# Kernel tuning notes

Hardware: AMD Instinct MI355X
Metric: run time of the kernel (lower is better)

The kernel has to match this reference:

```python
import jax, jax.numpy as jnp
import numpy as np

N_HEAD = 16


def setup_inputs() -> dict:
    key = jax.random.key(0)
    ks = jax.random.split(key, 6)
    B, T, C = 8, 1024, 1024
    s = 0.02
    return {
        "x": jax.random.normal(ks[0], (B, T, C), dtype=jnp.float32),
        "Wk": jax.random.normal(ks[1], (C, C), dtype=jnp.float32) * s,
        "bk": jnp.zeros((C,), dtype=jnp.float32),
        "Wq": jax.random.normal(ks[2], (C, C), dtype=jnp.float32) * s,
        "bq": jnp.zeros((C,), dtype=jnp.float32),
        "Wv": jax.random.normal(ks[3], (C, C), dtype=jnp.float32) * s,
        "bv": jnp.zeros((C,), dtype=jnp.float32),
        "Wp": jax.random.normal(ks[4], (C, C), dtype=jnp.float32) * s,
        "bp": jnp.zeros((C,), dtype=jnp.float32),
    }


def reference(x, Wk, bk, Wq, bq, Wv, bv, Wp, bp):
    B, T, C = x.shape
    H = N_HEAD
    d = C // H
    # QKV projections, split heads -> [B, H, T, d]
    k = (x @ Wk + bk).reshape(B, T, H, d).transpose(0, 2, 1, 3)
    q = (x @ Wq + bq).reshape(B, T, H, d).transpose(0, 2, 1, 3)
    v = (x @ Wv + bv).reshape(B, T, H, d).transpose(0, 2, 1, 3)
    # NOTE: original computes K @ Q^T (not Q @ K^T) and scales by C^-0.5
    attn = jnp.einsum('bhid,bhjd->bhij', k, q) * (C ** -0.5)
    mask = jnp.tril(jnp.ones((T, T), dtype=bool))  # tril==0 positions masked
    attn = jnp.where(mask, attn, -jnp.inf)
    attn = jax.nn.softmax(attn, axis=-1)
    out = jnp.einsum('bhij,bhjd->bhid', attn, v)  # [B, H, T, d]
    out = out.transpose(0, 2, 1, 3).reshape(B, T, C)
    return out @ Wp + bp
```

## Files before the change

### kernel.cpp

```cpp
#include <hip/hip_runtime.h>

typedef unsigned short u16;
typedef unsigned int u32;
typedef __bf16 bf16x8 __attribute__((ext_vector_type(8)));
typedef float f32x4 __attribute__((ext_vector_type(4)));

__device__ __forceinline__ u16 f2bf(float f) {
  u32 u = __builtin_bit_cast(u32, f);
  u += 0x7fffu + ((u >> 16) & 1u);
  return (u16)(u >> 16);
}

#define GLOAD_LDS16(g, l) __builtin_amdgcn_global_load_lds( \
    (const __attribute__((address_space(1))) void*)(g),     \
    (__attribute__((address_space(3))) void*)(l), 16, 0, 0)

#define SCK (0.03125f * 1.44269504088896f)

#define BARF() do { asm volatile("" ::: "memory"); \
                    __builtin_amdgcn_s_barrier();  \
                    asm volatile("" ::: "memory"); } while (0)

__global__ __launch_bounds__(256) void prep_k(const float* __restrict__ x,
                                              const float* __restrict__ W0,
                                              const float* __restrict__ W1,
                                              const float* __restrict__ W2,
                                              const float* __restrict__ W3,
                                              u16* __restrict__ xb,
                                              u16* __restrict__ WT) {
  __shared__ float tile[64][65];
  const int tid = threadIdx.x;
  if (blockIdx.x < 4096) {
    size_t i = (size_t)blockIdx.x * 256 + tid;
    const float4* p = reinterpret_cast<const float4*>(x) + i * 2;
    float4 a = p[0], b = p[1];
    u32 w0 = f2bf(a.x) | ((u32)f2bf(a.y) << 16);
    u32 w1 = f2bf(a.z) | ((u32)f2bf(a.w) << 16);
    u32 w2 = f2bf(b.x) | ((u32)f2bf(b.y) << 16);
    u32 w3 = f2bf(b.z) | ((u32)f2bf(b.w) << 16);
    uint4 o; o.x = w0; o.y = w1; o.z = w2; o.w = w3;
    *reinterpret_cast<uint4*>(xb + i * 8) = o;
    return;
  }
  const int bid2 = blockIdx.x - 4096;
  const int z = bid2 >> 8, kt = bid2 & 15, nt = (bid2 >> 4) & 15;
  const float* W = z == 0 ? W0 : z == 1 ? W1 : z == 2 ? W2 : W3;
  u16* dst = WT + (size_t)z * 1024 * 1024;
  const int k0 = kt * 64, n0 = nt * 64;
  const int rr = tid >> 4, c4 = (tid & 15) * 4;
#pragma unroll
  for (int p = 0; p < 4; ++p) {
    int r = rr + p * 16;
    float4 v = *reinterpret_cast<const float4*>(W + (size_t)(k0 + r) * 1024 + n0 + c4);
    tile[r][c4 + 0] = v.x; tile[r][c4 + 1] = v.y;
    tile[r][c4 + 2] = v.z; tile[r][c4 + 3] = v.w;
  }
  __syncthreads();
#pragma unroll
  for (int p = 0; p < 4; ++p) {
    int nl = rr + p * 16;
    u32 w0 = f2bf(tile[c4 + 0][nl]) | ((u32)f2bf(tile[c4 + 1][nl]) << 16);
    u32 w1 = f2bf(tile[c4 + 2][nl]) | ((u32)f2bf(tile[c4 + 3][nl]) << 16);
    uint2 o; o.x = w0; o.y = w1;
    *reinterpret_cast<uint2*>(dst + (size_t)(n0 + nl) * 1024 + k0 + c4) = o;
  }
}

template <int MODE>
__global__ __launch_bounds__(512, 2) void gemm8_k(
    const u16* __restrict__ A, const u16* __restrict__ BT,
    const float* __restrict__ bias0, const float* __restrict__ bias1,
    const float* __restrict__ bias2,
    u16* __restrict__ out_k, u16* __restrict__ out_q, u16* __restrict__ out_vT,
    float* __restrict__ out_f) {
  constexpr int BN = (MODE == 0) ? 192 : 128;
  constexpr int NB = BN / 64;
  constexpr int LPT = 4 + NB;
  constexpr int WCW = BN / 4;
  constexpr int HALF = 8 + NB;

  __shared__ __align__(16) u16 As[2][256 * 64];
  __shared__ __align__(16) u16 Bs[2][BN * 64];

  const int tid = threadIdx.x;
  const int w = tid >> 6, lane = tid & 63;
  const int wr = w >> 2, wc = w & 3;
  const int fr = lane & 15, fq = lane >> 4;
  const int d = fr & 7;

  const int bid = (int)blockIdx.x;
  const int xcd = bid & 7, c = bid >> 3;
  int bx, by;
  if constexpr (MODE == 0) {
    bx = (xcd & 3) * 8 + (c >> 3);
    by = (xcd >> 2) * 8 + (c & 7);
  } else {
    bx = xcd * 4 + (c >> 3);
    by = c & 7;
  }
  const int row0 = bx * 256, col0 = by * BN;

  const int r0 = tid >> 3;
  const int cbg = (tid & 7) ^ (r0 & 7);
  const u16* Asrc = A + (size_t)(row0 + r0) * 1024 + cbg * 8;
  const u16* Bsrc = BT + (size_t)(col0 + r0) * 1024 + cbg * 8;

#define STAGE8(buf, t) do {                                                  \
    _Pragma("unroll")                                                        \
    for (int sw = 0; sw < 4; ++sw)                                           \
      GLOAD_LDS16(Asrc + (size_t)sw * 65536 + (t) * 64,                      \
                  &As[buf][sw * 4096 + tid * 8]);                            \
    _Pragma("unroll")                                                        \
    for (int sw = 0; sw < NB; ++sw)                                          \
      GLOAD_LDS16(Bsrc + (size_t)sw * 65536 + (t) * 64,                      \
                  &Bs[buf][sw * 4096 + tid * 8]);                            \
  } while (0)

#define AOFF(mb, kk) ((wr * 128 + (mb) * 16 + fr) * 128 + (((((kk) << 2) | fq) ^ d) << 4))
#define BOFF(nb, kk) ((wc * WCW + (nb) * 16 + fr) * 128 + (((((kk) << 2) | fq) ^ d) << 4))

  f32x4 acc[8][NB] = {};

  STAGE8(0, 0);
  STAGE8(1, 1);
  asm volatile("s_waitcnt vmcnt(%0)" :: "n"(LPT) : "memory");
  BARF();

#pragma unroll 1
  for (int g = 0; g < 16; ++g) {
    const int buf = g & 1;
    const char* Ac = (const char*)&As[buf][0];
    const char* Bc = (const char*)&Bs[buf][0];
    bf16x8 a[8][2], b[NB][2];

#pragma unroll
    for (int mb = 0; mb < 8; ++mb) a[mb][0] = *(const bf16x8*)(Ac + AOFF(mb, 0));
#pragma unroll
    for (int nb = 0; nb < NB; ++nb) b[nb][0] = *(const bf16x8*)(Bc + BOFF(nb, 0));
#pragma unroll
    for (int mb = 0; mb < 8; ++mb) a[mb][1] = *(const bf16x8*)(Ac + AOFF(mb, 1));
#pragma unroll
    for (int nb = 0; nb < NB; ++nb) b[nb][1] = *(const bf16x8*)(Bc + BOFF(nb, 1));

    asm volatile("s_waitcnt lgkmcnt(%0)" :: "n"(HALF) : "memory");
    __builtin_amdgcn_s_setprio(1);
#pragma unroll
    for (int mb = 0; mb < 8; ++mb)
#pragma unroll
      for (int nb = 0; nb < NB; ++nb)
        acc[mb][nb] = __builtin_amdgcn_mfma_f32_16x16x32_bf16(
            a[mb][0], b[nb][0], acc[mb][nb], 0, 0, 0);
    __builtin_amdgcn_s_setprio(0);

    asm volatile("s_waitcnt lgkmcnt(0)" ::: "memory");
    BARF();
    if (g + 2 < 16) STAGE8(buf, g + 2);

    __builtin_amdgcn_s_setprio(1);
#pragma unroll
    for (int mb = 0; mb < 8; ++mb)
#pragma unroll
      for (int nb = 0; nb < NB; ++nb)
        acc[mb][nb] = __builtin_amdgcn_mfma_f32_16x16x32_bf16(
            a[mb][1], b[nb][1], acc[mb][nb], 0, 0, 0);
    __builtin_amdgcn_s_setprio(0);

    if (g <= 13)      asm volatile("s_waitcnt vmcnt(%0)" :: "n"(LPT) : "memory");
    else if (g == 14) asm volatile("s_waitcnt vmcnt(0)" ::: "memory");
    BARF();
  }
#undef STAGE8
#undef AOFF
#undef BOFF

  if constexpr (MODE == 0) {
#pragma unroll
    for (int mb = 0; mb < 8; ++mb) {
#pragma unroll
      for (int nb = 0; nb < NB; ++nb) {
        const int rg = row0 + wr * 128 + mb * 16 + fq * 4;
        const int cg = col0 + wc * WCW + nb * 16 + fr;
        const int which = cg >> 10;
        const int nloc = cg & 1023;
        const float bv = (which == 0 ? bias0 : which == 1 ? bias1 : bias2)[nloc];
        if (which == 0) {
#pragma unroll
          for (int r = 0; r < 4; ++r)
            out_k[(size_t)(rg + r) * 1024 + nloc] = f2bf((acc[mb][nb][r] + bv) * SCK);
        } else if (which == 1) {
#pragma unroll
          for (int r = 0; r < 4; ++r)
            out_q[(size_t)(rg + r) * 1024 + nloc] = f2bf(acc[mb][nb][r] + bv);
        } else {
          const int bb = rg >> 10, t = rg & 1023;
          const int hh = nloc >> 6, dl = nloc & 63;
          u32 w0 = f2bf(acc[mb][nb][0] + bv) | ((u32)f2bf(acc[mb][nb][1] + bv) << 16);
          u32 w1 = f2bf(acc[mb][nb][2] + bv) | ((u32)f2bf(acc[mb][nb][3] + bv) << 16);
          uint2 ov; ov.x = w0; ov.y = w1;
          *reinterpret_cast<uint2*>(out_vT + ((size_t)(bb * 16 + hh) * 64 + dl) * 1024 + t) = ov;
        }
      }
    }
  } else {
#pragma unroll
    for (int mb = 0; mb < 8; ++mb)
#pragma unroll
      for (int nb = 0; nb < NB; ++nb) {
        const int rg = row0 + wr * 128 + mb * 16 + fq * 4;
        const int cg = col0 + wc * WCW + nb * 16 + fr;
        const float bv = bias0[cg];
#pragma unroll
        for (int r = 0; r < 4; ++r)
          out_f[(size_t)(rg + r) * 1024 + cg] = acc[mb][nb][r] + bv;
      }
  }
}

__global__ __launch_bounds__(256, 4) void attn_k(const u16* __restrict__ Q,
                                                 const u16* __restrict__ K,
                                                 const u16* __restrict__ vT,
                                                 u16* __restrict__ O) {
  __shared__ __align__(16) u16 KsA[4096], KsB[4096], VsA[4096], VsB[4096];
  __shared__ __align__(16) u16 Plds[4][16][40];
  const int tid = threadIdx.x;
  const int w = tid >> 6, lane = tid & 63;
  const int fr = lane & 15, fq = lane >> 4, koff = fq * 8;

  const int n = blockIdx.x + 8 * (blockIdx.y + 16 * blockIdx.z);
  const int xcd = n & 7, rest = n >> 3;
  const int g = rest >> 3, pair = rest & 7;
  const int hb = xcd + 8 * g;
  const int h = hb & 15, b = hb >> 4;

  const size_t bstride = (size_t)1024 * 1024;
  const u16* Qb = Q + b * bstride + h * 64;
  const u16* Kg = K + b * bstride + h * 64;
  const u16* Vg = vT + ((size_t)(b * 16 + h) * 64) * 1024;

  const int srow = tid >> 3;
  const int scb = (tid & 7) ^ (srow & 7);
  const u16* KgT = Kg + (size_t)srow * 1024 + scb * 8;
  const u16* VgT = Vg + (size_t)srow * 1024 + scb * 8;

  const int vK0 = fr * 128 + ((fq ^ (fr & 7)) << 4);
  const int vK1 = vK0 ^ 64;
  const int pw = w * 1280 + fq * 320 + fr * 2;
  const int pr = w * 1280 + fr * 80 + fq * 16;

#define STAGE(KS, VS, jt) do {                                          \
    GLOAD_LDS16(KgT + (size_t)(jt) * 65536, &KS[tid * 8]);              \
    GLOAD_LDS16(KgT + (size_t)(jt) * 65536 + 32 * 1024, &KS[2048 + tid * 8]); \
    GLOAD_LDS16(VgT + (jt) * 64, &VS[tid * 8]);                         \
    GLOAD_LDS16(VgT + (jt) * 64 + 32 * 1024, &VS[2048 + tid * 8]);      \
  } while (0)

#pragma unroll 1
  for (int ph = 0; ph < 2; ++ph) {
    const int T = ph ? (15 - pair) : pair;
    const int i0 = T * 64;
    const int ibase = i0 + w * 16;

    bf16x8 aq0 = *reinterpret_cast<const bf16x8*>(&Qb[(size_t)(ibase + fr) * 1024 + koff]);
    bf16x8 aq1 = *reinterpret_cast<const bf16x8*>(&Qb[(size_t)(ibase + fr) * 1024 + koff + 32]);

    f32x4 o[4] = {};
    float lp[4] = {0.f, 0.f, 0.f, 0.f};

    auto compute = [&](const u16* KS, const u16* VS, bool diag) {
      const char* Kc = reinterpret_cast<const char*>(KS);
      const char* Vc = reinterpret_cast<const char*>(VS);
      f32x4 s[4];
#pragma unroll
      for (int jc = 0; jc < 4; ++jc) {
        bf16x8 bk0 = *reinterpret_cast<const bf16x8*>(Kc + vK0 + jc * 2048);
        bf16x8 bk1 = *reinterpret_cast<const bf16x8*>(Kc + vK1 + jc * 2048);
        f32x4 z = {};
        z = __builtin_amdgcn_mfma_f32_16x16x32_bf16(aq0, bk0, z, 0, 0, 0);
        s[jc] = __builtin_amdgcn_mfma_f32_16x16x32_bf16(aq1, bk1, z, 0, 0, 0);
      }
      bf16x8 bv0[4], bv1[4];
#pragma unroll
      for (int dn = 0; dn < 4; ++dn) {
        bv0[dn] = *reinterpret_cast<const bf16x8*>(Vc + vK0 + dn * 2048);
        bv1[dn] = *reinterpret_cast<const bf16x8*>(Vc + vK1 + dn * 2048);
      }
      float p[4][4];
      if (diag) {
#pragma unroll
        for (int r = 0; r < 4; ++r) {
          const int il = w * 16 + fq * 4 + r;
#pragma unroll
          for (int jc = 0; jc < 4; ++jc) {
            const int jl = jc * 16 + fr;
            p[jc][r] = (jl <= il) ? __builtin_amdgcn_exp2f(s[jc][r]) : 0.f;
          }
        }
      } else {
#pragma unroll
        for (int r = 0; r < 4; ++r)
#pragma unroll
          for (int jc = 0; jc < 4; ++jc)
            p[jc][r] = __builtin_amdgcn_exp2f(s[jc][r]);
      }
#pragma unroll
      for (int r = 0; r < 4; ++r)
        lp[r] += (p[0][r] + p[1][r]) + (p[2][r] + p[3][r]);
      char* Pc = reinterpret_cast<char*>(&Plds[0][0][0]);
#pragma unroll
      for (int jh = 0; jh < 2; ++jh) {
#pragma unroll
        for (int r = 0; r < 4; ++r)
#pragma unroll
          for (int j2 = 0; j2 < 2; ++j2)
            *reinterpret_cast<u16*>(Pc + pw + r * 80 + j2 * 32) = f2bf(p[jh * 2 + j2][r]);
        bf16x8 ap = *reinterpret_cast<const bf16x8*>(Pc + pr);
#pragma unroll
        for (int dn = 0; dn < 4; ++dn)
          o[dn] = __builtin_amdgcn_mfma_f32_16x16x32_bf16(ap, jh ? bv1[dn] : bv0[dn],
                                                          o[dn], 0, 0, 0);
      }
    };

    STAGE(KsA, VsA, 0);
    int t = 0;
    while (true) {
      {
        const bool more = t < T;
        if (more) STAGE(KsB, VsB, t + 1);
        if (more) { asm volatile("s_waitcnt vmcnt(4)" ::: "memory"); }
        else      { asm volatile("s_waitcnt vmcnt(0)" ::: "memory"); }
        __builtin_amdgcn_s_barrier();
        compute(KsA, VsA, t == T);
        __builtin_amdgcn_s_barrier();
        if (!more) break;
        ++t;
      }
      {
        const bool more = t < T;
        if (more) STAGE(KsA, VsA, t + 1);
        if (more) { asm volatile("s_waitcnt vmcnt(4)" ::: "memory"); }
        else      { asm volatile("s_waitcnt vmcnt(0)" ::: "memory"); }
        __builtin_amdgcn_s_barrier();
        compute(KsB, VsB, t == T);
        __builtin_amdgcn_s_barrier();
        if (!more) break;
        ++t;
      }
    }

#pragma unroll
    for (int x = 1; x < 16; x <<= 1)
#pragma unroll
      for (int r = 0; r < 4; ++r) lp[r] += __shfl_xor(lp[r], x);
#pragma unroll
    for (int r = 0; r < 4; ++r) {
      const float inv = 1.f / lp[r];
      const int ig = ibase + fq * 4 + r;
#pragma unroll
      for (int dn = 0; dn < 4; ++dn)
        O[((size_t)b * 1024 + ig) * 1024 + h * 64 + dn * 16 + fr] = f2bf(o[dn][r] * inv);
    }
  }
#undef STAGE
}

extern "C" void kernel_launch(void* const* d_in, const int* in_sizes, int n_in,
                              void* d_out, int out_size, void* d_ws, size_t ws_size,
                              hipStream_t stream) {
  const float* x  = (const float*)d_in[0];
  const float* Wk = (const float*)d_in[1];
  const float* bk = (const float*)d_in[2];
  const float* Wq = (const float*)d_in[3];
  const float* bq = (const float*)d_in[4];
  const float* Wv = (const float*)d_in[5];
  const float* bv = (const float*)d_in[6];
  const float* Wp = (const float*)d_in[7];
  const float* bp = (const float*)d_in[8];
  float* out = (float*)d_out;

  char* ws = (char*)d_ws;
  u16* xb   = (u16*)(ws);
  u16* WT   = (u16*)(ws + ((size_t)16 << 20));
  u16* kbuf = (u16*)(ws + ((size_t)24 << 20));
  u16* qbuf = (u16*)(ws + ((size_t)40 << 20));
  u16* vT   = (u16*)(ws + ((size_t)56 << 20));
  u16* aout = (u16*)(ws + ((size_t)72 << 20));

  prep_k<<<5120, 256, 0, stream>>>(x, Wk, Wq, Wv, Wp, xb, WT);
  gemm8_k<0><<<512, 512, 0, stream>>>(xb, WT, bk, bq, bv,
                                      kbuf, qbuf, vT, nullptr);
  attn_k<<<dim3(8, 16, 8), 256, 0, stream>>>(kbuf, qbuf, vT, aout);
  gemm8_k<1><<<256, 512, 0, stream>>>(aout, WT + (size_t)3 * 1024 * 1024,
                                      bp, nullptr, nullptr,
                                      nullptr, nullptr, nullptr, out);
}
```

Baseline: 132.7 us.

## Load K/V tiles directly from global into registers, drop LDS double-buffering

The attention kernel no longer stages K and V tiles into shared memory with async global-to-LDS loads and barriers. Each wave now reads its K and V fragments straight from global memory into registers, with no block-level synchronisation. The occupancy hint goes from 4 to 6 blocks per CU, which the smaller shared-memory footprint allows. The cost is that the four waves in a block each fetch the same K/V data separately (relying on cache), and the loads are no longer software-pipelined ahead of compute.

```diff
diff --git a/kernel.cpp b/kernel.cpp
--- a/kernel.cpp
+++ b/kernel.cpp
@@ -216,11 +216,10 @@
   }
 }
 
-__global__ __launch_bounds__(256, 4) void attn_k(const u16* __restrict__ Q,
+__global__ __launch_bounds__(256, 6) void attn_k(const u16* __restrict__ Q,
                                                  const u16* __restrict__ K,
                                                  const u16* __restrict__ vT,
                                                  u16* __restrict__ O) {
-  __shared__ __align__(16) u16 KsA[4096], KsB[4096], VsA[4096], VsB[4096];
   __shared__ __align__(16) u16 Plds[4][16][40];
   const int tid = threadIdx.x;
   const int w = tid >> 6, lane = tid & 63;
@@ -234,25 +233,12 @@
 
   const size_t bstride = (size_t)1024 * 1024;
   const u16* Qb = Q + b * bstride + h * 64;
-  const u16* Kg = K + b * bstride + h * 64;
-  const u16* Vg = vT + ((size_t)(b * 16 + h) * 64) * 1024;
-
-  const int srow = tid >> 3;
-  const int scb = (tid & 7) ^ (srow & 7);
-  const u16* KgT = Kg + (size_t)srow * 1024 + scb * 8;
-  const u16* VgT = Vg + (size_t)srow * 1024 + scb * 8;
-
-  const int vK0 = fr * 128 + ((fq ^ (fr & 7)) << 4);
-  const int vK1 = vK0 ^ 64;
+  const u16* Kb = K + b * bstride + h * 64;
+  const u16* Vb = vT + ((size_t)(b * 16 + h) * 64) * 1024;
+
   const int pw = w * 1280 + fq * 320 + fr * 2;
   const int pr = w * 1280 + fr * 80 + fq * 16;
-
-#define STAGE(KS, VS, jt) do {                                          \
-    GLOAD_LDS16(KgT + (size_t)(jt) * 65536, &KS[tid * 8]);              \
-    GLOAD_LDS16(KgT + (size_t)(jt) * 65536 + 32 * 1024, &KS[2048 + tid * 8]); \
-    GLOAD_LDS16(VgT + (jt) * 64, &VS[tid * 8]);                         \
-    GLOAD_LDS16(VgT + (jt) * 64 + 32 * 1024, &VS[2048 + tid * 8]);      \
-  } while (0)
+  char* Pc = reinterpret_cast<char*>(&Plds[0][0][0]);
 
 #pragma unroll 1
   for (int ph = 0; ph < 2; ++ph) {
@@ -266,26 +252,33 @@
     f32x4 o[4] = {};
     float lp[4] = {0.f, 0.f, 0.f, 0.f};
 
-    auto compute = [&](const u16* KS, const u16* VS, bool diag) {
-      const char* Kc = reinterpret_cast<const char*>(KS);
-      const char* Vc = reinterpret_cast<const char*>(VS);
+#pragma unroll 1
+    for (int j0 = 0; j0 <= i0; j0 += 64) {
+      bf16x8 bk0[4], bk1[4];
+#pragma unroll
+      for (int jc = 0; jc < 4; ++jc) {
+        const size_t kr = (size_t)(j0 + jc * 16 + fr) * 1024;
+        bk0[jc] = *reinterpret_cast<const bf16x8*>(&Kb[kr + koff]);
+        bk1[jc] = *reinterpret_cast<const bf16x8*>(&Kb[kr + koff + 32]);
+      }
+      bf16x8 bv[2][4];
+#pragma unroll
+      for (int kk = 0; kk < 2; ++kk)
+#pragma unroll
+        for (int dn = 0; dn < 4; ++dn)
+          bv[kk][dn] = *reinterpret_cast<const bf16x8*>(
+              &Vb[(size_t)(dn * 16 + fr) * 1024 + j0 + kk * 32 + koff]);
+
       f32x4 s[4];
 #pragma unroll
       for (int jc = 0; jc < 4; ++jc) {
-        bf16x8 bk0 = *reinterpret_cast<const bf16x8*>(Kc + vK0 + jc * 2048);
-        bf16x8 bk1 = *reinterpret_cast<const bf16x8*>(Kc + vK1 + jc * 2048);
         f32x4 z = {};
-        z = __builtin_amdgcn_mfma_f32_16x16x32_bf16(aq0, bk0, z, 0, 0, 0);
-        s[jc] = __builtin_amdgcn_mfma_f32_16x16x32_bf16(aq1, bk1, z, 0, 0, 0);
-      }
-      bf16x8 bv0[4], bv1[4];
-#pragma unroll
-      for (int dn = 0; dn < 4; ++dn) {
-        bv0[dn] = *reinterpret_cast<const bf16x8*>(Vc + vK0 + dn * 2048);
-        bv1[dn] = *reinterpret_cast<const bf16x8*>(Vc + vK1 + dn * 2048);
-      }
+        z = __builtin_amdgcn_mfma_f32_16x16x32_bf16(aq0, bk0[jc], z, 0, 0, 0);
+        s[jc] = __builtin_amdgcn_mfma_f32_16x16x32_bf16(aq1, bk1[jc], z, 0, 0, 0);
+      }
+
       float p[4][4];
-      if (diag) {
+      if (j0 == i0) {
 #pragma unroll
         for (int r = 0; r < 4; ++r) {
           const int il = w * 16 + fq * 4 + r;
@@ -305,7 +298,7 @@
 #pragma unroll
       for (int r = 0; r < 4; ++r)
         lp[r] += (p[0][r] + p[1][r]) + (p[2][r] + p[3][r]);
-      char* Pc = reinterpret_cast<char*>(&Plds[0][0][0]);
+
 #pragma unroll
       for (int jh = 0; jh < 2; ++jh) {
 #pragma unroll
@@ -316,35 +309,7 @@
         bf16x8 ap = *reinterpret_cast<const bf16x8*>(Pc + pr);
 #pragma unroll
         for (int dn = 0; dn < 4; ++dn)
-          o[dn] = __builtin_amdgcn_mfma_f32_16x16x32_bf16(ap, jh ? bv1[dn] : bv0[dn],
-                                                          o[dn], 0, 0, 0);
-      }
-    };
-
-    STAGE(KsA, VsA, 0);
-    int t = 0;
-    while (true) {
-      {
-        const bool more = t < T;
-        if (more) STAGE(KsB, VsB, t + 1);
-        if (more) { asm volatile("s_waitcnt vmcnt(4)" ::: "memory"); }
-        else      { asm volatile("s_waitcnt vmcnt(0)" ::: "memory"); }
-        __builtin_amdgcn_s_barrier();
-        compute(KsA, VsA, t == T);
-        __builtin_amdgcn_s_barrier();
-        if (!more) break;
-        ++t;
-      }
-      {
-        const bool more = t < T;
-        if (more) STAGE(KsA, VsA, t + 1);
-        if (more) { asm volatile("s_waitcnt vmcnt(4)" ::: "memory"); }
-        else      { asm volatile("s_waitcnt vmcnt(0)" ::: "memory"); }
-        __builtin_amdgcn_s_barrier();
-        compute(KsB, VsB, t == T);
-        __builtin_amdgcn_s_barrier();
-        if (!more) break;
-        ++t;
+          o[dn] = __builtin_amdgcn_mfma_f32_16x16x32_bf16(ap, bv[jh][dn], o[dn], 0, 0, 0);
       }
     }
 
@@ -361,7 +326,6 @@
         O[((size_t)b * 1024 + ig) * 1024 + h * 64 + dn * 16 + fr] = f2bf(o[dn][r] * inv);
     }
   }
-#undef STAGE
 }
 
 extern "C" void kernel_launch(void* const* d_in, const int* in_sizes, int n_in,
```

After: 228.1 us. +71.9%, slower.

## Replace output projection GEMM with dedicated 128x128-tile double-buffered kernel

Applied to the files above, without the earlier changes.

Swaps the generic gemm8 kernel for the final projection with a new projg_k kernel using 128x128 tiles, 256 threads, and 512 blocks instead of 256. The kernel double-buffers LDS via direct global-to-LDS loads with an XOR swizzle, interleaves MFMA halves with the next stage's loads, and remaps blocks per XCD for L2 locality. The aim is better occupancy and fill of the 256 CUs on this smaller GEMM, at the cost of less operand reuse per tile.

```diff
diff --git a/kernel.cpp b/kernel.cpp
--- a/kernel.cpp
+++ b/kernel.cpp
@@ -216,6 +216,110 @@
   }
 }
 
+__global__ __launch_bounds__(256, 2) void projg_k(const u16* __restrict__ A,
+                                                  const u16* __restrict__ BT,
+                                                  const float* __restrict__ bias,
+                                                  float* __restrict__ out_f) {
+  __shared__ __align__(16) u16 As[2][128 * 64];
+  __shared__ __align__(16) u16 Bs[2][128 * 64];
+
+  const int tid = threadIdx.x;
+  const int w = tid >> 6, lane = tid & 63;
+  const int wr = w >> 1, wc = w & 1;
+  const int fr = lane & 15, fq = lane >> 4;
+  const int d = fr & 7;
+
+  const int bid = (int)blockIdx.x;
+  const int xcd = bid & 7, c = bid >> 3;
+  const int bx = xcd * 8 + (c >> 3);
+  const int by = c & 7;
+  const int row0 = bx * 128, col0 = by * 128;
+
+  const int r0 = tid >> 3;
+  const int cbg = (tid & 7) ^ (r0 & 7);
+  const u16* Asrc = A + (size_t)(row0 + r0) * 1024 + cbg * 8;
+  const u16* Bsrc = BT + (size_t)(col0 + r0) * 1024 + cbg * 8;
+
+#define STAGEP(buf, t) do {                                                  \
+    _Pragma("unroll")                                                        \
+    for (int sw = 0; sw < 4; ++sw) {                                         \
+      GLOAD_LDS16(Asrc + (size_t)sw * 32768 + (t) * 64,                      \
+                  &As[buf][sw * 2048 + tid * 8]);                            \
+      GLOAD_LDS16(Bsrc + (size_t)sw * 32768 + (t) * 64,                      \
+                  &Bs[buf][sw * 2048 + tid * 8]);                            \
+    }                                                                        \
+  } while (0)
+
+#define APOFF(mb, kk) ((wr * 64 + (mb) * 16 + fr) * 128 + (((((kk) << 2) | fq) ^ d) << 4))
+#define BPOFF(nb, kk) ((wc * 64 + (nb) * 16 + fr) * 128 + (((((kk) << 2) | fq) ^ d) << 4))
+
+  f32x4 acc[4][4] = {};
+
+  STAGEP(0, 0);
+  STAGEP(1, 1);
+  asm volatile("s_waitcnt vmcnt(8)" ::: "memory");
+  BARF();
+
+#pragma unroll 1
+  for (int g = 0; g < 16; ++g) {
+    const int buf = g & 1;
+    const char* Ac = (const char*)&As[buf][0];
+    const char* Bc = (const char*)&Bs[buf][0];
+    bf16x8 a[4][2], b[4][2];
+
+#pragma unroll
+    for (int mb = 0; mb < 4; ++mb) a[mb][0] = *(const bf16x8*)(Ac + APOFF(mb, 0));
+#pragma unroll
+    for (int nb = 0; nb < 4; ++nb) b[nb][0] = *(const bf16x8*)(Bc + BPOFF(nb, 0));
+#pragma unroll
+    for (int mb = 0; mb < 4; ++mb) a[mb][1] = *(const bf16x8*)(Ac + APOFF(mb, 1));
+#pragma unroll
+    for (int nb = 0; nb < 4; ++nb) b[nb][1] = *(const bf16x8*)(Bc + BPOFF(nb, 1));
+
+    asm volatile("s_waitcnt lgkmcnt(8)" ::: "memory");
+    __builtin_amdgcn_s_setprio(1);
+#pragma unroll
+    for (int mb = 0; mb < 4; ++mb)
+#pragma unroll
+      for (int nb = 0; nb < 4; ++nb)
+        acc[mb][nb] = __builtin_amdgcn_mfma_f32_16x16x32_bf16(
+            a[mb][0], b[nb][0], acc[mb][nb], 0, 0, 0);
+    __builtin_amdgcn_s_setprio(0);
+
+    asm volatile("s_waitcnt lgkmcnt(0)" ::: "memory");
+    BARF();
+    if (g + 2 < 16) STAGEP(buf, g + 2);
+
+    __builtin_amdgcn_s_setprio(1);
+#pragma unroll
+    for (int mb = 0; mb < 4; ++mb)
+#pragma unroll
+      for (int nb = 0; nb < 4; ++nb)
+        acc[mb][nb] = __builtin_amdgcn_mfma_f32_16x16x32_bf16(
+            a[mb][1], b[nb][1], acc[mb][nb], 0, 0, 0);
+    __builtin_amdgcn_s_setprio(0);
+
+    if (g <= 13)      asm volatile("s_waitcnt vmcnt(8)" ::: "memory");
+    else if (g == 14) asm volatile("s_waitcnt vmcnt(0)" ::: "memory");
+    BARF();
+  }
+#undef STAGEP
+#undef APOFF
+#undef BPOFF
+
+#pragma unroll
+  for (int mb = 0; mb < 4; ++mb)
+#pragma unroll
+    for (int nb = 0; nb < 4; ++nb) {
+      const int rg = row0 + wr * 64 + mb * 16 + fq * 4;
+      const int cg = col0 + wc * 64 + nb * 16 + fr;
+      const float bv = bias[cg];
+#pragma unroll
+      for (int r = 0; r < 4; ++r)
+        out_f[(size_t)(rg + r) * 1024 + cg] = acc[mb][nb][r] + bv;
+    }
+}
+
 __global__ __launch_bounds__(256, 4) void attn_k(const u16* __restrict__ Q,
                                                  const u16* __restrict__ K,
                                                  const u16* __restrict__ vT,
@@ -390,7 +494,5 @@
   gemm8_k<0><<<512, 512, 0, stream>>>(xb, WT, bk, bq, bv,
                                       kbuf, qbuf, vT, nullptr);
   attn_k<<<dim3(8, 16, 8), 256, 0, stream>>>(kbuf, qbuf, vT, aout);
-  gemm8_k<1><<<256, 512, 0, stream>>>(aout, WT + (size_t)3 * 1024 * 1024,
-                                      bp, nullptr, nullptr,
-                                      nullptr, nullptr, nullptr, out);
-}
+  projg_k<<<512, 256, 0, stream>>>(aout, WT + (size_t)3 * 1024 * 1024, bp, out);
+}
```

Result: no change. 130.4 us (-1.7%).
